# Optimization experiments

Measured on AMD Instinct MI355X. Metric: run time of the kernel, lower is better.

The kernel has to match this reference:

```python
import jax, jax.numpy as jnp
import numpy as np

IN_SIZE = 512
OUT_SIZE = 256
HIDDEN = 256
LN_EPS = 1e-5


def setup_inputs() -> dict:
    key = jax.random.key(0)
    ks = jax.random.split(key, 9)
    B, S, K = 8, 2048, 16
    net_in = jax.random.normal(ks[0], (B, S, K, IN_SIZE), dtype=jnp.float32)
    embeds = jax.random.normal(ks[1], (B, S, OUT_SIZE), dtype=jnp.float32)
    m = jax.random.uniform(ks[2], (B, S, K, 1), dtype=jnp.float32)
    W1 = jax.random.normal(ks[3], (IN_SIZE, HIDDEN), dtype=jnp.float32) * 0.02
    b1 = jnp.full((HIDDEN,), 0.02, dtype=jnp.float32)
    Wf = jax.random.normal(ks[4], (HIDDEN, OUT_SIZE + 1), dtype=jnp.float32) * 0.02
    bf = jnp.zeros((OUT_SIZE + 1,), dtype=jnp.float32)
    gamma = jnp.ones((OUT_SIZE,), dtype=jnp.float32)
    beta = jnp.zeros((OUT_SIZE,), dtype=jnp.float32)
    return {"net_in": net_in, "embeds": embeds, "m": m, "W1": W1, "b1": b1,
            "Wf": Wf, "bf": bf, "gamma": gamma, "beta": beta}


def reference(net_in, embeds, m, W1, b1, Wf, bf, gamma, beta):
    # MLP: one hidden relu layer, final linear to out_size+1
    h = jax.nn.relu(jnp.einsum('bski,ih->bskh', net_in, W1) + b1)
    out = jnp.einsum('bskh,ho->bsko', h, Wf) + bf          # [B,S,K,out+1]
    # sigmoid on last channel (link weight), then mask
    out = jnp.concatenate([out[..., :-1], jax.nn.sigmoid(out[..., -1:])], axis=-1)
    out = m * out
    link_weight = out[..., -1] + 1e-8                       # [B,S,K]
    norm = jnp.sum(link_weight, axis=2, keepdims=True)      # [B,S,1]
    weights = (link_weight / norm)[..., None]               # [B,S,K,1]
    updates = jnp.sum(out * weights, axis=2)                # [B,S,out+1]
    # residual update
    upd_weights = updates[..., -1:]
    embeds_new = embeds + upd_weights * updates[..., :-1]
    # LayerNorm over last dim
    mu = jnp.mean(embeds_new, axis=-1, keepdims=True)
    var = jnp.var(embeds_new, axis=-1, keepdims=True)
    return (embeds_new - mu) * jax.lax.rsqrt(var + LN_EPS) * gamma + beta
```

## Files before the change

### kernel.cpp

```cpp
#include <hip/hip_runtime.h>

typedef short s16x8 __attribute__((ext_vector_type(8)));
typedef float f32x4 __attribute__((ext_vector_type(4)));

__device__ __forceinline__ unsigned short f2bf(float f) {
    union { float f; unsigned u; } v; v.f = f;
    return (unsigned short)((v.u + 0x7FFFu + ((v.u >> 16) & 1u)) >> 16);
}
__device__ __forceinline__ float bf2f(unsigned short h) {
    union { unsigned u; float f; } v; v.u = ((unsigned)h) << 16;
    return v.f;
}

__device__ __forceinline__ void wg_barrier_lds() {
    __builtin_amdgcn_sched_barrier(0);
    asm volatile("s_waitcnt lgkmcnt(0)" ::: "memory");
    __builtin_amdgcn_s_barrier();
    __builtin_amdgcn_sched_barrier(0);
}

#define NBLK 2048

__global__ void prep_weights(const float* __restrict__ W1, const float* __restrict__ Wf,
                             unsigned short* __restrict__ W1T, unsigned short* __restrict__ WfT) {
    int t = blockIdx.x * 256 + threadIdx.x;
    {
        int c  = t >> 13;
        int n  = (t >> 5) & 255;
        int kk = t & 31;
        W1T[t] = f2bf(W1[(c * 32 + kk) * 256 + n]);
    }
    if (t < 65536) {
        int c  = t >> 13;
        int n  = (t >> 5) & 255;
        int hh = t & 31;
        WfT[t] = f2bf(Wf[(c * 32 + hh) * 257 + n]);
    }
}

__global__ __launch_bounds__(512, 2)
void fused_embed(const float* __restrict__ net_in, const float* __restrict__ embeds,
                 const float* __restrict__ mg, const float* __restrict__ W1,
                 const float* __restrict__ b1, const float* __restrict__ Wf,
                 const float* __restrict__ bfv, const float* __restrict__ gam,
                 const float* __restrict__ bet, float* __restrict__ out,
                 const unsigned short* __restrict__ W1T, const unsigned short* __restrict__ WfT)
{
    __shared__ unsigned short Abuf[2][128][32];
    __shared__ unsigned short Hbuf[128][260];
    __shared__ unsigned short gbuf[16][264];
    __shared__ float updb[8][264];
    __shared__ float sbuf[8];

    const int tid  = threadIdx.x;
    const int lane = tid & 63;
    const int wid  = tid >> 6;
    const int wr   = wid >> 2;
    const int wc   = wid & 3;
    const int l15  = lane & 15;
    const int g8   = (lane >> 4) * 8;
    const int blk  = blockIdx.x;
    const int row0 = blk * 128;

    const f32x4 zero4 = {0.f, 0.f, 0.f, 0.f};

    f32x4 acc[4][4];
    #pragma unroll
    for (int i = 0; i < 4; ++i)
        #pragma unroll
        for (int j = 0; j < 4; ++j)
            acc[i][j] = zero4;

    const int ar = tid >> 2;
    const int ac = (tid & 3) * 8;
    const int wbase = (wc * 64 + l15) * 32 + g8;

    float4 vaA[6], vbA[6];
    s16x8  wW[2][8];

#define A_ISSUE(KC, S) do { \
        const float* _src = &net_in[(row0 + ar) * 512 + (KC) * 32 + ac]; \
        vaA[S] = *(const float4*)_src; \
        vbA[S] = *(const float4*)(_src + 4); \
    } while (0)

#define W_ISSUE(KC, S) do { \
        const unsigned short* _wp = W1T + (KC) * 8192 + wbase; \
        wW[S][0] = *(const s16x8*)(_wp); \
        wW[S][1] = *(const s16x8*)(_wp + 512); \
        wW[S][2] = *(const s16x8*)(_wp + 1024); \
        wW[S][3] = *(const s16x8*)(_wp + 1536); \
        wW[S][4] = *(const s16x8*)(_wp + 2048); \
        wW[S][5] = *(const s16x8*)(_wp + 2560); \
        wW[S][6] = *(const s16x8*)(_wp + 3072); \
        wW[S][7] = *(const s16x8*)(_wp + 3584); \
    } while (0)

#define A_WRITE(KC, S) do { \
        int4 _pk; \
        asm("v_cvt_pk_bf16_f32 %0, %1, %2" : "=v"(_pk.x) : "v"(vaA[S].x), "v"(vaA[S].y)); \
        asm("v_cvt_pk_bf16_f32 %0, %1, %2" : "=v"(_pk.y) : "v"(vaA[S].z), "v"(vaA[S].w)); \
        asm("v_cvt_pk_bf16_f32 %0, %1, %2" : "=v"(_pk.z) : "v"(vbA[S].x), "v"(vbA[S].y)); \
        asm("v_cvt_pk_bf16_f32 %0, %1, %2" : "=v"(_pk.w) : "v"(vbA[S].z), "v"(vbA[S].w)); \
        *(int4*)&Abuf[(KC) & 1][ar][ac] = _pk; \
    } while (0)

    A_ISSUE(0, 0); A_ISSUE(1, 1); A_ISSUE(2, 2);
    A_ISSUE(3, 3); A_ISSUE(4, 4); A_ISSUE(5, 5);
    W_ISSUE(0, 0);
    W_ISSUE(1, 1);
    A_WRITE(0, 0);
    wg_barrier_lds();

    #pragma unroll
    for (int kc = 0; kc < 16; ++kc) {
        const int cur = kc & 1;
        s16x8 b0 = wW[cur][0], b1r = wW[cur][1], b2 = wW[cur][2], b3 = wW[cur][3];
        if (kc < 10) A_ISSUE(kc + 6, kc % 6);
        if (kc < 14) W_ISSUE(kc + 2, cur);
        if (kc < 15) A_WRITE(kc + 1, (kc + 1) % 6);
        s16x8 af[4];
        #pragma unroll
        for (int i = 0; i < 4; ++i)
            af[i] = *(const s16x8*)&Abuf[cur][(wr * 4 + i) * 16 + l15][g8];
        #pragma unroll
        for (int i = 0; i < 4; ++i) {
            acc[i][0] = __builtin_amdgcn_mfma_f32_16x16x32_bf16(af[i], b0, acc[i][0], 0, 0, 0);
            acc[i][1] = __builtin_amdgcn_mfma_f32_16x16x32_bf16(af[i], b1r, acc[i][1], 0, 0, 0);
            acc[i][2] = __builtin_amdgcn_mfma_f32_16x16x32_bf16(af[i], b2, acc[i][2], 0, 0, 0);
            acc[i][3] = __builtin_amdgcn_mfma_f32_16x16x32_bf16(af[i], b3, acc[i][3], 0, 0, 0);
        }
        wg_barrier_lds();
    }
#undef A_ISSUE
#undef W_ISSUE
#undef A_WRITE

    #pragma unroll
    for (int j = 0; j < 4; ++j) {
        int col = wc * 64 + j * 16 + l15;
        float bb = b1[col];
        #pragma unroll
        for (int i = 0; i < 4; ++i) {
            #pragma unroll
            for (int r = 0; r < 4; ++r) {
                int row = (wr * 4 + i) * 16 + (lane >> 4) * 4 + r;
                Hbuf[row][col] = f2bf(fmaxf(acc[i][j][r] + bb, 0.f));
            }
        }
    }
    __syncthreads();

    float wl0 = Wf[(lane * 4 + 0) * 257 + 256];
    float wl1 = Wf[(lane * 4 + 1) * 257 + 256];
    float wl2 = Wf[(lane * 4 + 2) * 257 + 256];
    float wl3 = Wf[(lane * 4 + 3) * 257 + 256];
    float bf256 = bfv[256];

    float lcreg = 0.f;
    for (int k = 0; k < 16; ++k) {
        ushort4 hv = *(const ushort4*)&Hbuf[wid * 16 + k][lane * 4];
        float p = bf2f(hv.x) * wl0 + bf2f(hv.y) * wl1 + bf2f(hv.z) * wl2 + bf2f(hv.w) * wl3;
        #pragma unroll
        for (int off = 32; off > 0; off >>= 1) p += __shfl_xor(p, off, 64);
        if (lane == k) lcreg = p;
    }

    float wwreg = 0.f;
    float u256 = 0.f;
    if (lane < 16) {
        float mv  = mg[(blk * 8 + wid) * 16 + lane];
        float raw = lcreg + bf256;
        float sg  = 1.f / (1.f + expf(-raw));
        float v   = mv * sg;
        float lw  = v + 1e-8f;
        float nrm = lw;
        #pragma unroll
        for (int off = 8; off > 0; off >>= 1) nrm += __shfl_xor(nrm, off, 16);
        float wk = lw / nrm;
        wwreg = wk * mv;
        float u = wk * v;
        float s = wwreg;
        #pragma unroll
        for (int off = 8; off > 0; off >>= 1) {
            u += __shfl_xor(u, off, 16);
            s += __shfl_xor(s, off, 16);
        }
        u256 = u;
        if (lane == 0) sbuf[wid] = s;
    }
    u256 = __shfl(u256, 0, 64);

    {
        float ga0 = 0.f, ga1 = 0.f, ga2 = 0.f, ga3 = 0.f;
        #pragma unroll
        for (int k = 0; k < 16; ++k) {
            float wwk = __shfl(wwreg, k, 64);
            ushort4 hv = *(const ushort4*)&Hbuf[wid * 16 + k][lane * 4];
            ga0 += wwk * bf2f(hv.x);
            ga1 += wwk * bf2f(hv.y);
            ga2 += wwk * bf2f(hv.z);
            ga3 += wwk * bf2f(hv.w);
        }
        ushort4 gw; gw.x = f2bf(ga0); gw.y = f2bf(ga1); gw.z = f2bf(ga2); gw.w = f2bf(ga3);
        *(ushort4*)&gbuf[wid][lane * 4] = gw;
        ushort4 z4; z4.x = 0; z4.y = 0; z4.z = 0; z4.w = 0;
        *(ushort4*)&gbuf[8 + wid][lane * 4] = z4;
    }
    __syncthreads();

    f32x4 acc2[2];
    acc2[0] = zero4; acc2[1] = zero4;
    {
        const int w2n0 = ((wid * 2 + 0) * 16 + l15) * 32 + g8;
        const int w2n1 = ((wid * 2 + 1) * 16 + l15) * 32 + g8;
        s16x8 w2a[2], w2b[2];
        w2a[0] = *(const s16x8*)(WfT + w2n0);
        w2b[0] = *(const s16x8*)(WfT + w2n1);
        #pragma unroll
        for (int c2 = 0; c2 < 8; ++c2) {
            const int cur = c2 & 1;
            s16x8 ba = w2a[cur], bb = w2b[cur];
            if (c2 < 7) {
                w2a[cur ^ 1] = *(const s16x8*)(WfT + (c2 + 1) * 8192 + w2n0);
                w2b[cur ^ 1] = *(const s16x8*)(WfT + (c2 + 1) * 8192 + w2n1);
            }
            s16x8 ga = *(const s16x8*)&gbuf[l15][c2 * 32 + g8];
            acc2[0] = __builtin_amdgcn_mfma_f32_16x16x32_bf16(ga, ba, acc2[0], 0, 0, 0);
            acc2[1] = __builtin_amdgcn_mfma_f32_16x16x32_bf16(ga, bb, acc2[1], 0, 0, 0);
        }
    }

    {
        int gq = lane >> 4;
        if (gq < 2) {
            #pragma unroll
            for (int t = 0; t < 2; ++t) {
                int col = (wid * 2 + t) * 16 + l15;
                float bfc = bfv[col];
                #pragma unroll
                for (int r = 0; r < 4; ++r) {
                    int p = gq * 4 + r;
                    updb[p][col] = acc2[t][r] + sbuf[p] * bfc;
                }
            }
        }
    }
    __syncthreads();

    {
        int base = (blk * 8 + wid) * 256;
        float4 up = *(const float4*)&updb[wid][lane * 4];
        float4 em = *(const float4*)&embeds[base + lane * 4];
        float e0 = em.x + u256 * up.x;
        float e1 = em.y + u256 * up.y;
        float e2 = em.z + u256 * up.z;
        float e3 = em.w + u256 * up.w;
        float s1 = e0 + e1 + e2 + e3;
        float s2 = e0 * e0 + e1 * e1 + e2 * e2 + e3 * e3;
        #pragma unroll
        for (int off = 32; off > 0; off >>= 1) {
            s1 += __shfl_xor(s1, off, 64);
            s2 += __shfl_xor(s2, off, 64);
        }
        float mu  = s1 * (1.f / 256.f);
        float var = s2 * (1.f / 256.f) - mu * mu;
        float rs  = rsqrtf(var + 1e-5f);
        float4 gm = *(const float4*)&gam[lane * 4];
        float4 bt = *(const float4*)&bet[lane * 4];
        float4 o;
        o.x = (e0 - mu) * rs * gm.x + bt.x;
        o.y = (e1 - mu) * rs * gm.y + bt.y;
        o.z = (e2 - mu) * rs * gm.z + bt.z;
        o.w = (e3 - mu) * rs * gm.w + bt.w;
        *(float4*)&out[base + lane * 4] = o;
    }
}

extern "C" void kernel_launch(void* const* d_in, const int* in_sizes, int n_in,
                              void* d_out, int out_size, void* d_ws, size_t ws_size,
                              hipStream_t stream) {
    (void)in_sizes; (void)n_in; (void)ws_size; (void)out_size;
    const float* net_in = (const float*)d_in[0];
    const float* embeds = (const float*)d_in[1];
    const float* mg     = (const float*)d_in[2];
    const float* W1     = (const float*)d_in[3];
    const float* b1     = (const float*)d_in[4];
    const float* Wf     = (const float*)d_in[5];
    const float* bfv    = (const float*)d_in[6];
    const float* gam    = (const float*)d_in[7];
    const float* bet    = (const float*)d_in[8];
    float* outp = (float*)d_out;

    unsigned short* W1T = (unsigned short*)d_ws;
    unsigned short* WfT = W1T + 131072;

    prep_weights<<<512, 256, 0, stream>>>(W1, Wf, W1T, WfT);
    fused_embed<<<NBLK, 512, 0, stream>>>(net_in, embeds, mg, W1, b1, Wf, bfv, gam, bet, outp, W1T, WfT);
}
```

Measured before the change: 205.3 us.

## Process two K-chunks per barrier with 4-deep LDS ring and rotated chunk order

```diff
diff --git a/kernel.cpp b/kernel.cpp
--- a/kernel.cpp
+++ b/kernel.cpp
@@ -46,7 +46,7 @@
                  const float* __restrict__ bet, float* __restrict__ out,
                  const unsigned short* __restrict__ W1T, const unsigned short* __restrict__ WfT)
 {
-    __shared__ unsigned short Abuf[2][128][32];
+    __shared__ unsigned short Abuf[4][128][32];
     __shared__ unsigned short Hbuf[128][260];
     __shared__ unsigned short gbuf[16][264];
     __shared__ float updb[8][264];
@@ -61,6 +61,7 @@
     const int g8   = (lane >> 4) * 8;
     const int blk  = blockIdx.x;
     const int row0 = blk * 128;
+    const int rc   = blk & 15;
 
     const f32x4 zero4 = {0.f, 0.f, 0.f, 0.f};
 
@@ -76,59 +77,74 @@
     const int wbase = (wc * 64 + l15) * 32 + g8;
 
     float4 vaA[6], vbA[6];
-    s16x8  wW[2][8];
-
-#define A_ISSUE(KC, S) do { \
-        const float* _src = &net_in[(row0 + ar) * 512 + (KC) * 32 + ac]; \
+    s16x8  wW[4][4];
+
+#define A_ISSUE(C, S) do { \
+        const int _pc = ((C) + rc) & 15; \
+        const float* _src = &net_in[(row0 + ar) * 512 + _pc * 32 + ac]; \
         vaA[S] = *(const float4*)_src; \
         vbA[S] = *(const float4*)(_src + 4); \
     } while (0)
 
-#define W_ISSUE(KC, S) do { \
-        const unsigned short* _wp = W1T + (KC) * 8192 + wbase; \
+#define W_ISSUE(C, S) do { \
+        const int _pc = ((C) + rc) & 15; \
+        const unsigned short* _wp = W1T + _pc * 8192 + wbase; \
         wW[S][0] = *(const s16x8*)(_wp); \
         wW[S][1] = *(const s16x8*)(_wp + 512); \
         wW[S][2] = *(const s16x8*)(_wp + 1024); \
         wW[S][3] = *(const s16x8*)(_wp + 1536); \
-        wW[S][4] = *(const s16x8*)(_wp + 2048); \
-        wW[S][5] = *(const s16x8*)(_wp + 2560); \
-        wW[S][6] = *(const s16x8*)(_wp + 3072); \
-        wW[S][7] = *(const s16x8*)(_wp + 3584); \
     } while (0)
 
-#define A_WRITE(KC, S) do { \
+#define A_WRITE(C, S) do { \
         int4 _pk; \
         asm("v_cvt_pk_bf16_f32 %0, %1, %2" : "=v"(_pk.x) : "v"(vaA[S].x), "v"(vaA[S].y)); \
         asm("v_cvt_pk_bf16_f32 %0, %1, %2" : "=v"(_pk.y) : "v"(vaA[S].z), "v"(vaA[S].w)); \
         asm("v_cvt_pk_bf16_f32 %0, %1, %2" : "=v"(_pk.z) : "v"(vbA[S].x), "v"(vbA[S].y)); \
         asm("v_cvt_pk_bf16_f32 %0, %1, %2" : "=v"(_pk.w) : "v"(vbA[S].z), "v"(vbA[S].w)); \
-        *(int4*)&Abuf[(KC) & 1][ar][ac] = _pk; \
+        *(int4*)&Abuf[(C) & 3][ar][ac] = _pk; \
     } while (0)
 
     A_ISSUE(0, 0); A_ISSUE(1, 1); A_ISSUE(2, 2);
     A_ISSUE(3, 3); A_ISSUE(4, 4); A_ISSUE(5, 5);
-    W_ISSUE(0, 0);
-    W_ISSUE(1, 1);
+    W_ISSUE(0, 0); W_ISSUE(1, 1); W_ISSUE(2, 2); W_ISSUE(3, 3);
     A_WRITE(0, 0);
+    A_WRITE(1, 1);
     wg_barrier_lds();
 
     #pragma unroll
-    for (int kc = 0; kc < 16; ++kc) {
-        const int cur = kc & 1;
-        s16x8 b0 = wW[cur][0], b1r = wW[cur][1], b2 = wW[cur][2], b3 = wW[cur][3];
-        if (kc < 10) A_ISSUE(kc + 6, kc % 6);
-        if (kc < 14) W_ISSUE(kc + 2, cur);
-        if (kc < 15) A_WRITE(kc + 1, (kc + 1) % 6);
-        s16x8 af[4];
-        #pragma unroll
-        for (int i = 0; i < 4; ++i)
-            af[i] = *(const s16x8*)&Abuf[cur][(wr * 4 + i) * 16 + l15][g8];
-        #pragma unroll
-        for (int i = 0; i < 4; ++i) {
-            acc[i][0] = __builtin_amdgcn_mfma_f32_16x16x32_bf16(af[i], b0, acc[i][0], 0, 0, 0);
-            acc[i][1] = __builtin_amdgcn_mfma_f32_16x16x32_bf16(af[i], b1r, acc[i][1], 0, 0, 0);
-            acc[i][2] = __builtin_amdgcn_mfma_f32_16x16x32_bf16(af[i], b2, acc[i][2], 0, 0, 0);
-            acc[i][3] = __builtin_amdgcn_mfma_f32_16x16x32_bf16(af[i], b3, acc[i][3], 0, 0, 0);
+    for (int t = 0; t < 8; ++t) {
+        const int c0 = 2 * t;
+        const int c1 = 2 * t + 1;
+        s16x8 b0 = wW[c0 & 3][0], b1r = wW[c0 & 3][1], b2 = wW[c0 & 3][2], b3 = wW[c0 & 3][3];
+        s16x8 d0 = wW[c1 & 3][0], d1 = wW[c1 & 3][1], d2 = wW[c1 & 3][2], d3 = wW[c1 & 3][3];
+        if (t < 5) { A_ISSUE(c0 + 6, (c0 + 6) % 6); A_ISSUE(c0 + 7, (c0 + 7) % 6); }
+        if (t < 6) { W_ISSUE(c0 + 4, c0 & 3); W_ISSUE(c0 + 5, c1 & 3); }
+        if (t < 7) { A_WRITE(c0 + 2, (c0 + 2) % 6); A_WRITE(c0 + 3, (c0 + 3) % 6); }
+        {
+            s16x8 af[4];
+            #pragma unroll
+            for (int i = 0; i < 4; ++i)
+                af[i] = *(const s16x8*)&Abuf[c0 & 3][(wr * 4 + i) * 16 + l15][g8];
+            #pragma unroll
+            for (int i = 0; i < 4; ++i) {
+                acc[i][0] = __builtin_amdgcn_mfma_f32_16x16x32_bf16(af[i], b0, acc[i][0], 0, 0, 0);
+                acc[i][1] = __builtin_amdgcn_mfma_f32_16x16x32_bf16(af[i], b1r, acc[i][1], 0, 0, 0);
+                acc[i][2] = __builtin_amdgcn_mfma_f32_16x16x32_bf16(af[i], b2, acc[i][2], 0, 0, 0);
+                acc[i][3] = __builtin_amdgcn_mfma_f32_16x16x32_bf16(af[i], b3, acc[i][3], 0, 0, 0);
+            }
+        }
+        {
+            s16x8 af[4];
+            #pragma unroll
+            for (int i = 0; i < 4; ++i)
+                af[i] = *(const s16x8*)&Abuf[c1 & 3][(wr * 4 + i) * 16 + l15][g8];
+            #pragma unroll
+            for (int i = 0; i < 4; ++i) {
+                acc[i][0] = __builtin_amdgcn_mfma_f32_16x16x32_bf16(af[i], d0, acc[i][0], 0, 0, 0);
+                acc[i][1] = __builtin_amdgcn_mfma_f32_16x16x32_bf16(af[i], d1, acc[i][1], 0, 0, 0);
+                acc[i][2] = __builtin_amdgcn_mfma_f32_16x16x32_bf16(af[i], d2, acc[i][2], 0, 0, 0);
+                acc[i][3] = __builtin_amdgcn_mfma_f32_16x16x32_bf16(af[i], d3, acc[i][3], 0, 0, 0);
+            }
         }
         wg_barrier_lds();
     }
```

New measurement: 209.2 us. No clear change (+1.9%).

## Stream net_in into LDS via direct global-to-LDS DMA with 4-stage ring

Applied to the files above, without the earlier changes.

```diff
diff --git a/kernel.cpp b/kernel.cpp
--- a/kernel.cpp
+++ b/kernel.cpp
@@ -12,11 +12,12 @@
     return v.f;
 }
 
-__device__ __forceinline__ void wg_barrier_lds() {
-    __builtin_amdgcn_sched_barrier(0);
-    asm volatile("s_waitcnt lgkmcnt(0)" ::: "memory");
-    __builtin_amdgcn_s_barrier();
-    __builtin_amdgcn_sched_barrier(0);
+typedef unsigned int u32;
+typedef const u32 __attribute__((address_space(1))) gu32;
+typedef u32 __attribute__((address_space(3))) lu32;
+
+__device__ __forceinline__ void gload16(const void* g, void* l) {
+    __builtin_amdgcn_global_load_lds((gu32*)g, (lu32*)l, 16, 0, 0);
 }
 
 #define NBLK 2048
@@ -46,7 +47,7 @@
                  const float* __restrict__ bet, float* __restrict__ out,
                  const unsigned short* __restrict__ W1T, const unsigned short* __restrict__ WfT)
 {
-    __shared__ unsigned short Abuf[2][128][32];
+    __shared__ float Abuf[4][128][32];
     __shared__ unsigned short Hbuf[128][260];
     __shared__ unsigned short gbuf[16][264];
     __shared__ float updb[8][264];
@@ -71,17 +72,20 @@
         for (int j = 0; j < 4; ++j)
             acc[i][j] = zero4;
 
-    const int ar = tid >> 2;
-    const int ac = (tid & 3) * 8;
     const int wbase = (wc * 64 + l15) * 32 + g8;
 
-    float4 vaA[6], vbA[6];
-    s16x8  wW[2][8];
-
-#define A_ISSUE(KC, S) do { \
-        const float* _src = &net_in[(row0 + ar) * 512 + (KC) * 32 + ac]; \
-        vaA[S] = *(const float4*)_src; \
-        vbA[S] = *(const float4*)(_src + 4); \
+    const int r0 = tid >> 3, c0 = tid & 7;
+    const int r1 = 64 + (tid >> 3);
+    const int sc0 = (c0 ^ (r0 & 7)) * 4;
+    const int sc1 = (c0 ^ (r1 & 7)) * 4;
+    char* const ldsbase = (char*)&Abuf[0][0][0];
+
+    s16x8 wW[2][4];
+
+#define A_DMA(KC) do { \
+        char* _d = ldsbase + ((KC) & 3) * 16384 + tid * 16; \
+        gload16(net_in + (size_t)(row0 + r0) * 512 + (KC) * 32 + sc0, _d); \
+        gload16(net_in + (size_t)(row0 + r1) * 512 + (KC) * 32 + sc1, _d + 8192); \
     } while (0)
 
 #define W_ISSUE(KC, S) do { \
@@ -90,51 +94,51 @@
         wW[S][1] = *(const s16x8*)(_wp + 512); \
         wW[S][2] = *(const s16x8*)(_wp + 1024); \
         wW[S][3] = *(const s16x8*)(_wp + 1536); \
-        wW[S][4] = *(const s16x8*)(_wp + 2048); \
-        wW[S][5] = *(const s16x8*)(_wp + 2560); \
-        wW[S][6] = *(const s16x8*)(_wp + 3072); \
-        wW[S][7] = *(const s16x8*)(_wp + 3584); \
     } while (0)
 
-#define A_WRITE(KC, S) do { \
-        int4 _pk; \
-        asm("v_cvt_pk_bf16_f32 %0, %1, %2" : "=v"(_pk.x) : "v"(vaA[S].x), "v"(vaA[S].y)); \
-        asm("v_cvt_pk_bf16_f32 %0, %1, %2" : "=v"(_pk.y) : "v"(vaA[S].z), "v"(vaA[S].w)); \
-        asm("v_cvt_pk_bf16_f32 %0, %1, %2" : "=v"(_pk.z) : "v"(vbA[S].x), "v"(vbA[S].y)); \
-        asm("v_cvt_pk_bf16_f32 %0, %1, %2" : "=v"(_pk.w) : "v"(vbA[S].z), "v"(vbA[S].w)); \
-        *(int4*)&Abuf[(KC) & 1][ar][ac] = _pk; \
-    } while (0)
-
-    A_ISSUE(0, 0); A_ISSUE(1, 1); A_ISSUE(2, 2);
-    A_ISSUE(3, 3); A_ISSUE(4, 4); A_ISSUE(5, 5);
     W_ISSUE(0, 0);
     W_ISSUE(1, 1);
-    A_WRITE(0, 0);
-    wg_barrier_lds();
+    A_DMA(0); A_DMA(1); A_DMA(2);
+    __builtin_amdgcn_sched_barrier(0);
+    asm volatile("s_waitcnt vmcnt(4)" ::: "memory");
+    __builtin_amdgcn_s_barrier();
+    __builtin_amdgcn_sched_barrier(0);
 
     #pragma unroll
     for (int kc = 0; kc < 16; ++kc) {
-        const int cur = kc & 1;
-        s16x8 b0 = wW[cur][0], b1r = wW[cur][1], b2 = wW[cur][2], b3 = wW[cur][3];
-        if (kc < 10) A_ISSUE(kc + 6, kc % 6);
-        if (kc < 14) W_ISSUE(kc + 2, cur);
-        if (kc < 15) A_WRITE(kc + 1, (kc + 1) % 6);
-        s16x8 af[4];
-        #pragma unroll
-        for (int i = 0; i < 4; ++i)
-            af[i] = *(const s16x8*)&Abuf[cur][(wr * 4 + i) * 16 + l15][g8];
+        const int slot = kc & 3;
+        s16x8 b0 = wW[kc & 1][0], b1r = wW[kc & 1][1], b2 = wW[kc & 1][2], b3 = wW[kc & 1][3];
+        if (kc < 14) W_ISSUE(kc + 2, kc & 1);
+        if (kc < 13) A_DMA(kc + 3);
         #pragma unroll
         for (int i = 0; i < 4; ++i) {
-            acc[i][0] = __builtin_amdgcn_mfma_f32_16x16x32_bf16(af[i], b0, acc[i][0], 0, 0, 0);
-            acc[i][1] = __builtin_amdgcn_mfma_f32_16x16x32_bf16(af[i], b1r, acc[i][1], 0, 0, 0);
-            acc[i][2] = __builtin_amdgcn_mfma_f32_16x16x32_bf16(af[i], b2, acc[i][2], 0, 0, 0);
-            acc[i][3] = __builtin_amdgcn_mfma_f32_16x16x32_bf16(af[i], b3, acc[i][3], 0, 0, 0);
-        }
-        wg_barrier_lds();
-    }
-#undef A_ISSUE
+            const int row = (wr * 4 + i) * 16 + l15;
+            const int gx = (lane >> 4) * 2;
+            f32x4 lo = *(const f32x4*)&Abuf[slot][row][((gx + 0) ^ (l15 & 7)) * 4];
+            f32x4 hi = *(const f32x4*)&Abuf[slot][row][((gx + 1) ^ (l15 & 7)) * 4];
+            int4 pk;
+            asm("v_cvt_pk_bf16_f32 %0, %1, %2" : "=v"(pk.x) : "v"(lo.x), "v"(lo.y));
+            asm("v_cvt_pk_bf16_f32 %0, %1, %2" : "=v"(pk.y) : "v"(lo.z), "v"(lo.w));
+            asm("v_cvt_pk_bf16_f32 %0, %1, %2" : "=v"(pk.z) : "v"(hi.x), "v"(hi.y));
+            asm("v_cvt_pk_bf16_f32 %0, %1, %2" : "=v"(pk.w) : "v"(hi.z), "v"(hi.w));
+            s16x8 af = *(const s16x8*)&pk;
+            acc[i][0] = __builtin_amdgcn_mfma_f32_16x16x32_bf16(af, b0, acc[i][0], 0, 0, 0);
+            acc[i][1] = __builtin_amdgcn_mfma_f32_16x16x32_bf16(af, b1r, acc[i][1], 0, 0, 0);
+            acc[i][2] = __builtin_amdgcn_mfma_f32_16x16x32_bf16(af, b2, acc[i][2], 0, 0, 0);
+            acc[i][3] = __builtin_amdgcn_mfma_f32_16x16x32_bf16(af, b3, acc[i][3], 0, 0, 0);
+        }
+        if (kc < 15) {
+            __builtin_amdgcn_sched_barrier(0);
+            if (kc == 0)       asm volatile("s_waitcnt vmcnt(8)"  ::: "memory");
+            else if (kc <= 12) asm volatile("s_waitcnt vmcnt(12)" ::: "memory");
+            else if (kc == 13) asm volatile("s_waitcnt vmcnt(10)" ::: "memory");
+            else               asm volatile("s_waitcnt vmcnt(4)"  ::: "memory");
+            __builtin_amdgcn_s_barrier();
+            __builtin_amdgcn_sched_barrier(0);
+        }
+    }
+#undef A_DMA
 #undef W_ISSUE
-#undef A_WRITE
 
     #pragma unroll
     for (int j = 0; j < 4; ++j) {
```

New measurement: 209.7 us. 1.02x slower.
